# Kernel optimization log

Measured on AMD Instinct MI355X. Metric: run time of the kernel, lower is better.

## Reference

```python
import jax, jax.numpy as jnp
import numpy as np

N = 100000        # nodes
E = 1600000       # edges (N * avg_degree 16)
D_IN = 128
D_OUT = 32
OBS_T = 60        # observation_time -> decay table size 60*OBS_T = 3600
T_MAX = 60 * OBS_T


def setup_inputs() -> dict:
    key = jax.random.key(0)
    ks = jax.random.split(key, 8)
    inp = {
        "input": jax.random.normal(ks[0], (N, D_IN), dtype=jnp.float32),
        "W": jax.random.normal(ks[1], (D_IN, D_OUT), dtype=jnp.float32) * (np.sqrt(2.0) / np.sqrt(D_IN)),
        # decay weights are abs(normal(0, 0.02)) in the original; rand*0.04 is same scale
        "decay_weight1": jnp.abs(jax.random.normal(ks[2], (T_MAX, 1), dtype=jnp.float32) * 0.02),
        "decay_weight2": jnp.abs(jax.random.normal(ks[3], (T_MAX, 1), dtype=jnp.float32) * 0.02),
        "edge_row": jax.random.randint(ks[4], (E,), 0, N, dtype=jnp.int32),
        "edge_col": jax.random.randint(ks[5], (E,), 0, N, dtype=jnp.int32),
        # zero-based interval index; equals (adj_value - 1) of the original code
        "edge_time": jax.random.randint(ks[6], (E,), 0, T_MAX, dtype=jnp.int32),
        "arrive_time": jax.random.randint(ks[7], (N,), 0, T_MAX, dtype=jnp.int32),
        "observation_time": OBS_T,
    }
    return inp


def reference(input, W, decay_weight1, decay_weight2,
              edge_row, edge_col, edge_time, arrive_time, observation_time):
    n_nodes = input.shape[0]
    # h = relu(input @ W)  [N, D_OUT]
    h = jax.nn.relu(jnp.matmul(input, W))
    # one-hot(interval) @ decay_weight1 == embedding lookup  -> per-edge decay scalar
    decay = decay_weight1[edge_time, 0]                        # [E]
    # SpecialSpmm: out[i] = sum_{edges (i,j)} decay_e * h[j]  (gather-scale-scatter)
    msgs = decay[:, None] * h[edge_col]                        # [E, D_OUT]
    h_prime = jax.ops.segment_sum(msgs, edge_row, num_segments=n_nodes)
    # outlayer window decay: one-hot(60*T - arrive - 1) @ decay_weight2 == lookup
    win_idx = 60 * observation_time - arrive_time - 1          # [N] in [0, 60*T)
    h_prime = decay_weight2[win_idx, 0][:, None] * h_prime
    return h_prime
```

## Files before the change

### kernel.cpp

```cpp
#include <hip/hip_runtime.h>

#define N_NODES 100000
#define N_EDGES 1600000
#define D_IN    128
#define D_OUT   32
#define CROWS   2048
#define NCB     49
#define NSH     8
#define NSEG    (NCB * NSH)
#define CAP_A   4500
#define DEPTH   48
#define SEGSTRIDE 4608
#define SSTRIDE 2064
#define CAPW    1024
#define RPB3    32
#define K3_BLKS (NCB * 64)
#define GEMM_BLKS ((N_NODES + 63) / 64)
#define GEMM_A  782
#define GEMM_B  (GEMM_BLKS - GEMM_A)
#define GRID_A  2048
#define EPB_A   ((N_EDGES + GRID_A - 1) / GRID_A)

typedef __attribute__((ext_vector_type(8))) short bf16x8;
typedef __attribute__((ext_vector_type(4))) float f32x4;

__device__ inline short f2bf(float f) {
    union { float f; unsigned u; } v; v.f = f;
    unsigned r = (v.u + 0x7FFFu + ((v.u >> 16) & 1u)) >> 16;
    return (short)r;
}

__device__ inline void gemm_role(const float* __restrict__ input,
                                 const float* __restrict__ W,
                                 unsigned short* __restrict__ h16,
                                 short* wbt, int gblk, int tid)
{
    for (int i = tid; i < D_IN * D_OUT; i += 256) {
        const int k = i >> 5, c = i & 31;
        wbt[c * D_IN + k] = f2bf(W[i]);
    }
    __syncthreads();

    const int wave = tid >> 6;
    const int lane = tid & 63;
    const int r0   = gblk * 64 + wave * 16;
    const int c16  = lane & 15;
    const int quad = lane >> 4;

    int ra = r0 + c16;
    if (ra >= N_NODES) ra = N_NODES - 1;
    const float* arow = input + (size_t)ra * D_IN;

    f32x4 acc0 = {0.f, 0.f, 0.f, 0.f};
    f32x4 acc1 = {0.f, 0.f, 0.f, 0.f};
#pragma unroll
    for (int q = 0; q < 4; ++q) {
        const float* ap = arow + q * 32 + quad * 8;
        f32x4 a0 = *(const f32x4*)(ap);
        f32x4 a1 = *(const f32x4*)(ap + 4);
        bf16x8 af;
        af[0] = f2bf(a0.x); af[1] = f2bf(a0.y); af[2] = f2bf(a0.z); af[3] = f2bf(a0.w);
        af[4] = f2bf(a1.x); af[5] = f2bf(a1.y); af[6] = f2bf(a1.z); af[7] = f2bf(a1.w);
        bf16x8 b0 = *(const bf16x8*)(wbt + (c16)      * D_IN + q * 32 + quad * 8);
        bf16x8 b1 = *(const bf16x8*)(wbt + (c16 + 16) * D_IN + q * 32 + quad * 8);
        acc0 = __builtin_amdgcn_mfma_f32_16x16x32_bf16(af, b0, acc0, 0, 0, 0);
        acc1 = __builtin_amdgcn_mfma_f32_16x16x32_bf16(af, b1, acc1, 0, 0, 0);
    }
#pragma unroll
    for (int i = 0; i < 4; ++i) {
        const int rr = r0 + quad * 4 + i;
        if (rr < N_NODES) {
            h16[(size_t)rr * D_OUT + c16]      = (unsigned short)f2bf(fmaxf(acc0[i], 0.f));
            h16[(size_t)rr * D_OUT + c16 + 16] = (unsigned short)f2bf(fmaxf(acc1[i], 0.f));
        }
    }
}

union SMemPAG {
    struct { uint2 lbin[NCB][DEPTH]; int lcnt[NCB]; int gbase[NCB]; } a;
    struct { short wbt[D_IN * D_OUT]; } g;
};

__global__ __launch_bounds__(256) void phaseA_gemmA_kernel(
    const float* __restrict__ input, const float* __restrict__ W,
    const int* __restrict__ erow,    const int* __restrict__ ecol,
    const int* __restrict__ etime,
    unsigned short* __restrict__ h16,
    int* __restrict__ gcur,
    uint2* __restrict__ segA)
{
    __shared__ SMemPAG sm;
    const int tid = threadIdx.x;

    if (blockIdx.x < GRID_A) {
        const int blk   = blockIdx.x;
        const int shard = blk & (NSH - 1);
        const int wv    = tid >> 6;
        const int ln    = tid & 63;

        if (tid < NCB) sm.a.lcnt[tid] = 0;
        __syncthreads();

        const int e_beg = blk * EPB_A;
        const int e_end = min(e_beg + EPB_A, N_EDGES);

        for (int e = e_beg + tid; e < e_end; e += 256) {
            const int row = erow[e];
            const int cb  = row >> 11;
            uint2 p;
            p.x = (unsigned)ecol[e] | ((unsigned)(row & (CROWS - 1)) << 17);
            p.y = (unsigned)etime[e];
            const int pos = atomicAdd(&sm.a.lcnt[cb], 1);
            if (pos < DEPTH) sm.a.lbin[cb][pos] = p;
            else {
                const int gp = atomicAdd(&gcur[(cb * NSH + shard) * 16], 1);
                if (gp < CAP_A) segA[(size_t)(cb * NSH + shard) * CAP_A + gp] = p;
            }
        }
        __syncthreads();

        if (tid < NCB) {
            const int c = min(sm.a.lcnt[tid], DEPTH);
            sm.a.gbase[tid] = atomicAdd(&gcur[(tid * NSH + shard) * 16], c);
        }
        __syncthreads();

        for (int bin = wv; bin < NCB; bin += 4) {
            const int c  = min(sm.a.lcnt[bin], DEPTH);
            const int gb = sm.a.gbase[bin];
            uint2* seg = segA + (size_t)(bin * NSH + shard) * CAP_A;
            for (int k = ln; k < c; k += 64)
                if (gb + k < CAP_A) seg[gb + k] = sm.a.lbin[bin][k];
        }
    } else {
        gemm_role(input, W, h16, sm.g.wbt, blockIdx.x - GRID_A, tid);
    }
}

union SMemSSG {
    struct { int hist[CROWS]; int curs[CROWS]; int part[256]; } s;
    struct { short wbt[D_IN * D_OUT]; } g;
};

__global__ __launch_bounds__(256) void sortseg_gemmB_kernel(
    const float* __restrict__ input, const float* __restrict__ W,
    unsigned short* __restrict__ h16,
    const int* __restrict__ gcur, const uint2* __restrict__ segA,
    int* __restrict__ sseg, unsigned* __restrict__ spk2s)
{
    __shared__ SMemSSG sm;
    const int tid = threadIdx.x;

    if (blockIdx.x < NSEG) {
        const int b = blockIdx.x;
        const int n = min(gcur[b * 16], CAP_A);
        const uint2* seg = segA + (size_t)b * CAP_A;

        for (int t = tid; t < CROWS; t += 256) sm.s.hist[t] = 0;
        __syncthreads();

        for (int i = tid; i < n; i += 256)
            atomicAdd(&sm.s.hist[(seg[i].x >> 17) & (CROWS - 1)], 1);
        __syncthreads();

        int tmp[8]; int s0 = 0;
        const int base = tid * 8;
#pragma unroll
        for (int k = 0; k < 8; ++k) { tmp[k] = sm.s.hist[base + k]; s0 += tmp[k]; }
        sm.s.part[tid] = s0;
        __syncthreads();
        for (int off = 1; off < 256; off <<= 1) {
            int v = sm.s.part[tid];
            if (tid >= off) v += sm.s.part[tid - off];
            __syncthreads(); sm.s.part[tid] = v; __syncthreads();
        }
        int run = sm.s.part[tid] - s0;
#pragma unroll
        for (int k = 0; k < 8; ++k) { sm.s.curs[base + k] = run; run += tmp[k]; }
        __syncthreads();

        int* sg = sseg + (size_t)b * SSTRIDE;
        for (int t = tid; t < CROWS; t += 256) sg[t] = sm.s.curs[t];
        if (tid == 0) sg[CROWS] = n;
        __syncthreads();

        unsigned* dst = spk2s + (size_t)b * SEGSTRIDE;
        for (int i = tid; i < n; i += 256) {
            const uint2 p  = seg[i];
            const int   rl = (p.x >> 17) & (CROWS - 1);
            dst[atomicAdd(&sm.s.curs[rl], 1)] = (p.x & 0x1FFFFu) | (p.y << 20);
        }
    } else {
        gemm_role(input, W, h16, sm.g.wbt, GEMM_A + (int)blockIdx.x - NSEG, tid);
    }
}

__global__ __launch_bounds__(256) void merge_reduce_kernel(
    const unsigned short* __restrict__ h16, const int* __restrict__ sseg,
    const unsigned* __restrict__ spk2s,
    const float* __restrict__ dw1, const float* __restrict__ dw2,
    const int* __restrict__ arrive, const int* __restrict__ obs,
    float* __restrict__ out)
{
    __shared__ int ls8[NSH][RPB3 + 1];
    __shared__ int pre[NSH][RPB3];
    __shared__ int totL[RPB3];
    __shared__ int dstart[RPB3 + 1];
    __shared__ unsigned st[CAPW];

    const int b   = blockIdx.x;
    const int cb  = b >> 6;
    const int rl0 = (b & 63) * RPB3;
    const int g0  = cb * CROWS + rl0;
    if (g0 >= N_NODES) return;
    const int tid = threadIdx.x;

    for (int t = tid; t < NSH * (RPB3 + 1); t += 256) {
        const int s = t / (RPB3 + 1), i = t - s * (RPB3 + 1);
        ls8[s][i] = sseg[(size_t)(cb * NSH + s) * SSTRIDE + rl0 + i];
    }
    __syncthreads();

    if (tid < RPB3) {
        int accp = 0;
#pragma unroll
        for (int s = 0; s < NSH; ++s) {
            pre[s][tid] = accp;
            accp += ls8[s][tid + 1] - ls8[s][tid];
        }
        totL[tid] = accp;
    }
    __syncthreads();
    if (tid == 0) {
        int runp = 0;
#pragma unroll
        for (int r = 0; r < RPB3; ++r) { dstart[r] = runp; runp += totL[r]; }
        dstart[RPB3] = runp;
    }
    __syncthreads();

#pragma unroll
    for (int s = 0; s < NSH; ++s) {
        const int sb   = ls8[s][0];
        const int span = ls8[s][RPB3] - sb;
        const unsigned* src = spk2s + (size_t)(cb * NSH + s) * SEGSTRIDE;
        for (int i = tid; i < span; i += 256) {
            const int gidx = sb + i;
            int lo = 0, hi = RPB3 - 1;
#pragma unroll
            for (int it = 0; it < 5; ++it) {
                const int mid = (lo + hi + 1) >> 1;
                if (ls8[s][mid] <= gidx) lo = mid; else hi = mid - 1;
            }
            const int pos = dstart[lo] + pre[s][lo] + (gidx - ls8[s][lo]);
            if (pos < CAPW) st[pos] = src[gidx];
        }
    }
    __syncthreads();

    const int g  = tid >> 3;
    const int li = tid & 7;
    const int row = g0 + g;
    const int begc = min(dstart[g], CAPW);
    const int endc = min(dstart[g + 1], CAPW);
    const int n    = endc - begc;
    const unsigned* recs = &st[begc];
    const unsigned short* hp = h16 + li * 4;

    float a0 = 0.f, a1 = 0.f, a2 = 0.f, a3 = 0.f;
    int j = 0;
    for (; j + 8 <= n; j += 8) {
#pragma unroll
        for (int u = 0; u < 8; ++u) {
            const unsigned rec = recs[j + u];
            const uint2 hv = *(const uint2*)(hp + ((size_t)(rec & 0x1FFFFu) << 5));
            const float w  = dw1[rec >> 20];
            a0 = fmaf(w, __uint_as_float(hv.x << 16),         a0);
            a1 = fmaf(w, __uint_as_float(hv.x & 0xFFFF0000u), a1);
            a2 = fmaf(w, __uint_as_float(hv.y << 16),         a2);
            a3 = fmaf(w, __uint_as_float(hv.y & 0xFFFF0000u), a3);
        }
    }
    for (; j < n; ++j) {
        const unsigned rec = recs[j];
        const uint2 hv = *(const uint2*)(hp + ((size_t)(rec & 0x1FFFFu) << 5));
        const float w  = dw1[rec >> 20];
        a0 = fmaf(w, __uint_as_float(hv.x << 16),         a0);
        a1 = fmaf(w, __uint_as_float(hv.x & 0xFFFF0000u), a1);
        a2 = fmaf(w, __uint_as_float(hv.y << 16),         a2);
        a3 = fmaf(w, __uint_as_float(hv.y & 0xFFFF0000u), a3);
    }

    const int T = 60 * obs[0];
    const float sdw = dw2[T - arrive[row] - 1];
    float4 o;
    o.x = a0 * sdw; o.y = a1 * sdw; o.z = a2 * sdw; o.w = a3 * sdw;
    *(float4*)(out + ((size_t)row << 5) + li * 4) = o;
}

extern "C" void kernel_launch(void* const* d_in, const int* in_sizes, int n_in,
                              void* d_out, int out_size, void* d_ws, size_t ws_size,
                              hipStream_t stream)
{
    const float* input  = (const float*)d_in[0];
    const float* W      = (const float*)d_in[1];
    const float* dw1    = (const float*)d_in[2];
    const float* dw2    = (const float*)d_in[3];
    const int*   erow   = (const int*)d_in[4];
    const int*   ecol   = (const int*)d_in[5];
    const int*   etime  = (const int*)d_in[6];
    const int*   arrive = (const int*)d_in[7];
    const int*   obs    = (const int*)d_in[8];

    float* out = (float*)d_out;

    char* p = (char*)d_ws;
    unsigned short* h16 = (unsigned short*)p;
    p += (size_t)N_NODES * D_OUT * 2;
    p = (char*)(((size_t)p + 255) & ~(size_t)255);
    int* gcur = (int*)p;
    p += (size_t)NSEG * 16 * 4;
    p = (char*)(((size_t)p + 255) & ~(size_t)255);
    uint2* segA = (uint2*)p;
    p += (size_t)NSEG * CAP_A * 8;
    p = (char*)(((size_t)p + 255) & ~(size_t)255);
    unsigned* spk2s = (unsigned*)p;
    p += (size_t)NSEG * SEGSTRIDE * 4;
    p = (char*)(((size_t)p + 255) & ~(size_t)255);
    int* sseg = (int*)p;

    hipMemsetAsync(gcur, 0, (size_t)NSEG * 16 * 4, stream);

    phaseA_gemmA_kernel<<<GRID_A + GEMM_A, 256, 0, stream>>>(
        input, W, erow, ecol, etime, h16, gcur, segA);
    sortseg_gemmB_kernel<<<NSEG + GEMM_B, 256, 0, stream>>>(
        input, W, h16, gcur, segA, sseg, spk2s);
    merge_reduce_kernel<<<K3_BLKS, 256, 0, stream>>>(
        h16, sseg, spk2s, dw1, dw2, arrive, obs, out);
}
```

Measured before the change: 176.2 us.

## Fuse sort and merge kernels with per-chunk atomic readiness flags

All GEMM blocks now run in the first kernel alongside binning, instead of splitting the GEMM across two kernels. The sort and merge kernels are merged into one launch: sort blocks signal completion per column-block chunk with release atomics, and merge blocks spin-wait on those counters before consuming the sorted segments. This removes one kernel launch boundary and lets merging of ready chunks overlap with sorting of others. In exchange it relies on sort blocks being scheduled before the dependent merge blocks, which could deadlock if they were not, and the spinning burns CU slots.

New measurement: 649.2 us. +268.4%, slower.

```diff
diff --git a/kernel.cpp b/kernel.cpp
--- a/kernel.cpp
+++ b/kernel.cpp
@@ -14,10 +14,8 @@
 #define SSTRIDE 2064
 #define CAPW    1024
 #define RPB3    32
-#define K3_BLKS (NCB * 64)
+#define MERGE_BLKS (NCB * 64)
 #define GEMM_BLKS ((N_NODES + 63) / 64)
-#define GEMM_A  782
-#define GEMM_B  (GEMM_BLKS - GEMM_A)
 #define GRID_A  2048
 #define EPB_A   ((N_EDGES + GRID_A - 1) / GRID_A)
 
@@ -30,58 +28,12 @@
     return (short)r;
 }
 
-__device__ inline void gemm_role(const float* __restrict__ input,
-                                 const float* __restrict__ W,
-                                 unsigned short* __restrict__ h16,
-                                 short* wbt, int gblk, int tid)
-{
-    for (int i = tid; i < D_IN * D_OUT; i += 256) {
-        const int k = i >> 5, c = i & 31;
-        wbt[c * D_IN + k] = f2bf(W[i]);
-    }
-    __syncthreads();
-
-    const int wave = tid >> 6;
-    const int lane = tid & 63;
-    const int r0   = gblk * 64 + wave * 16;
-    const int c16  = lane & 15;
-    const int quad = lane >> 4;
-
-    int ra = r0 + c16;
-    if (ra >= N_NODES) ra = N_NODES - 1;
-    const float* arow = input + (size_t)ra * D_IN;
-
-    f32x4 acc0 = {0.f, 0.f, 0.f, 0.f};
-    f32x4 acc1 = {0.f, 0.f, 0.f, 0.f};
-#pragma unroll
-    for (int q = 0; q < 4; ++q) {
-        const float* ap = arow + q * 32 + quad * 8;
-        f32x4 a0 = *(const f32x4*)(ap);
-        f32x4 a1 = *(const f32x4*)(ap + 4);
-        bf16x8 af;
-        af[0] = f2bf(a0.x); af[1] = f2bf(a0.y); af[2] = f2bf(a0.z); af[3] = f2bf(a0.w);
-        af[4] = f2bf(a1.x); af[5] = f2bf(a1.y); af[6] = f2bf(a1.z); af[7] = f2bf(a1.w);
-        bf16x8 b0 = *(const bf16x8*)(wbt + (c16)      * D_IN + q * 32 + quad * 8);
-        bf16x8 b1 = *(const bf16x8*)(wbt + (c16 + 16) * D_IN + q * 32 + quad * 8);
-        acc0 = __builtin_amdgcn_mfma_f32_16x16x32_bf16(af, b0, acc0, 0, 0, 0);
-        acc1 = __builtin_amdgcn_mfma_f32_16x16x32_bf16(af, b1, acc1, 0, 0, 0);
-    }
-#pragma unroll
-    for (int i = 0; i < 4; ++i) {
-        const int rr = r0 + quad * 4 + i;
-        if (rr < N_NODES) {
-            h16[(size_t)rr * D_OUT + c16]      = (unsigned short)f2bf(fmaxf(acc0[i], 0.f));
-            h16[(size_t)rr * D_OUT + c16 + 16] = (unsigned short)f2bf(fmaxf(acc1[i], 0.f));
-        }
-    }
-}
-
-union SMemPAG {
+union SMemGA {
+    struct { short wbt[D_IN * D_OUT]; } g;
     struct { uint2 lbin[NCB][DEPTH]; int lcnt[NCB]; int gbase[NCB]; } a;
-    struct { short wbt[D_IN * D_OUT]; } g;
 };
 
-__global__ __launch_bounds__(256) void phaseA_gemmA_kernel(
+__global__ __launch_bounds__(256) void gemm_phaseA_kernel(
     const float* __restrict__ input, const float* __restrict__ W,
     const int* __restrict__ erow,    const int* __restrict__ ecol,
     const int* __restrict__ etime,
@@ -89,11 +41,51 @@
     int* __restrict__ gcur,
     uint2* __restrict__ segA)
 {
-    __shared__ SMemPAG sm;
+    __shared__ SMemGA sm;
     const int tid = threadIdx.x;
 
-    if (blockIdx.x < GRID_A) {
-        const int blk   = blockIdx.x;
+    if (blockIdx.x < GEMM_BLKS) {
+        for (int i = tid; i < D_IN * D_OUT; i += 256) {
+            const int k = i >> 5, c = i & 31;
+            sm.g.wbt[c * D_IN + k] = f2bf(W[i]);
+        }
+        __syncthreads();
+
+        const int wave = tid >> 6;
+        const int lane = tid & 63;
+        const int r0   = blockIdx.x * 64 + wave * 16;
+        const int c16  = lane & 15;
+        const int quad = lane >> 4;
+
+        int ra = r0 + c16;
+        if (ra >= N_NODES) ra = N_NODES - 1;
+        const float* arow = input + (size_t)ra * D_IN;
+
+        f32x4 acc0 = {0.f, 0.f, 0.f, 0.f};
+        f32x4 acc1 = {0.f, 0.f, 0.f, 0.f};
+#pragma unroll
+        for (int q = 0; q < 4; ++q) {
+            const float* ap = arow + q * 32 + quad * 8;
+            f32x4 a0 = *(const f32x4*)(ap);
+            f32x4 a1 = *(const f32x4*)(ap + 4);
+            bf16x8 af;
+            af[0] = f2bf(a0.x); af[1] = f2bf(a0.y); af[2] = f2bf(a0.z); af[3] = f2bf(a0.w);
+            af[4] = f2bf(a1.x); af[5] = f2bf(a1.y); af[6] = f2bf(a1.z); af[7] = f2bf(a1.w);
+            bf16x8 b0 = *(const bf16x8*)(sm.g.wbt + (c16)      * D_IN + q * 32 + quad * 8);
+            bf16x8 b1 = *(const bf16x8*)(sm.g.wbt + (c16 + 16) * D_IN + q * 32 + quad * 8);
+            acc0 = __builtin_amdgcn_mfma_f32_16x16x32_bf16(af, b0, acc0, 0, 0, 0);
+            acc1 = __builtin_amdgcn_mfma_f32_16x16x32_bf16(af, b1, acc1, 0, 0, 0);
+        }
+#pragma unroll
+        for (int i = 0; i < 4; ++i) {
+            const int rr = r0 + quad * 4 + i;
+            if (rr < N_NODES) {
+                h16[(size_t)rr * D_OUT + c16]      = (unsigned short)f2bf(fmaxf(acc0[i], 0.f));
+                h16[(size_t)rr * D_OUT + c16 + 16] = (unsigned short)f2bf(fmaxf(acc1[i], 0.f));
+            }
+        }
+    } else {
+        const int blk   = blockIdx.x - GEMM_BLKS;
         const int shard = blk & (NSH - 1);
         const int wv    = tid >> 6;
         const int ln    = tid & 63;
@@ -132,23 +124,25 @@
             for (int k = ln; k < c; k += 64)
                 if (gb + k < CAP_A) seg[gb + k] = sm.a.lbin[bin][k];
         }
-    } else {
-        gemm_role(input, W, h16, sm.g.wbt, blockIdx.x - GRID_A, tid);
     }
 }
 
-union SMemSSG {
+union SMemSM {
     struct { int hist[CROWS]; int curs[CROWS]; int part[256]; } s;
-    struct { short wbt[D_IN * D_OUT]; } g;
+    struct { int ls8[NSH][RPB3 + 1]; int pre[NSH][RPB3]; int totL[RPB3];
+             int dstart[RPB3 + 1]; unsigned st[CAPW]; } m;
 };
 
-__global__ __launch_bounds__(256) void sortseg_gemmB_kernel(
-    const float* __restrict__ input, const float* __restrict__ W,
-    unsigned short* __restrict__ h16,
+__global__ __launch_bounds__(256) void sort_merge_kernel(
+    const unsigned short* __restrict__ h16,
     const int* __restrict__ gcur, const uint2* __restrict__ segA,
-    int* __restrict__ sseg, unsigned* __restrict__ spk2s)
+    int* __restrict__ sseg, unsigned* __restrict__ spk2s,
+    int* __restrict__ segdone,
+    const float* __restrict__ dw1, const float* __restrict__ dw2,
+    const int* __restrict__ arrive, const int* __restrict__ obs,
+    float* __restrict__ out)
 {
-    __shared__ SMemSSG sm;
+    __shared__ SMemSM sm;
     const int tid = threadIdx.x;
 
     if (blockIdx.x < NSEG) {
@@ -190,89 +184,95 @@
             const int   rl = (p.x >> 17) & (CROWS - 1);
             dst[atomicAdd(&sm.s.curs[rl], 1)] = (p.x & 0x1FFFFu) | (p.y << 20);
         }
+        __syncthreads();
+
+        if (tid == 0) {
+            __threadfence();
+            __hip_atomic_fetch_add(&segdone[(b >> 3) * 16], 1,
+                                   __ATOMIC_RELEASE, __HIP_MEMORY_SCOPE_AGENT);
+        }
     } else {
-        gemm_role(input, W, h16, sm.g.wbt, GEMM_A + (int)blockIdx.x - NSEG, tid);
-    }
-}
-
-__global__ __launch_bounds__(256) void merge_reduce_kernel(
-    const unsigned short* __restrict__ h16, const int* __restrict__ sseg,
-    const unsigned* __restrict__ spk2s,
-    const float* __restrict__ dw1, const float* __restrict__ dw2,
-    const int* __restrict__ arrive, const int* __restrict__ obs,
-    float* __restrict__ out)
-{
-    __shared__ int ls8[NSH][RPB3 + 1];
-    __shared__ int pre[NSH][RPB3];
-    __shared__ int totL[RPB3];
-    __shared__ int dstart[RPB3 + 1];
-    __shared__ unsigned st[CAPW];
-
-    const int b   = blockIdx.x;
-    const int cb  = b >> 6;
-    const int rl0 = (b & 63) * RPB3;
-    const int g0  = cb * CROWS + rl0;
-    if (g0 >= N_NODES) return;
-    const int tid = threadIdx.x;
-
-    for (int t = tid; t < NSH * (RPB3 + 1); t += 256) {
-        const int s = t / (RPB3 + 1), i = t - s * (RPB3 + 1);
-        ls8[s][i] = sseg[(size_t)(cb * NSH + s) * SSTRIDE + rl0 + i];
-    }
-    __syncthreads();
-
-    if (tid < RPB3) {
-        int accp = 0;
+        const int b2  = blockIdx.x - NSEG;
+        const int cb  = b2 >> 6;
+        const int rl0 = (b2 & 63) * RPB3;
+        const int g0  = cb * CROWS + rl0;
+        if (g0 >= N_NODES) return;
+
+        if (tid == 0) {
+            while (__hip_atomic_load(&segdone[cb * 16], __ATOMIC_ACQUIRE,
+                                     __HIP_MEMORY_SCOPE_AGENT) < NSH)
+                __builtin_amdgcn_s_sleep(2);
+        }
+        __syncthreads();
+
+        for (int t = tid; t < NSH * (RPB3 + 1); t += 256) {
+            const int s = t / (RPB3 + 1), i = t - s * (RPB3 + 1);
+            sm.m.ls8[s][i] = sseg[(size_t)(cb * NSH + s) * SSTRIDE + rl0 + i];
+        }
+        __syncthreads();
+
+        if (tid < RPB3) {
+            int accp = 0;
+#pragma unroll
+            for (int s = 0; s < NSH; ++s) {
+                sm.m.pre[s][tid] = accp;
+                accp += sm.m.ls8[s][tid + 1] - sm.m.ls8[s][tid];
+            }
+            sm.m.totL[tid] = accp;
+        }
+        __syncthreads();
+        if (tid == 0) {
+            int runp = 0;
+#pragma unroll
+            for (int r = 0; r < RPB3; ++r) { sm.m.dstart[r] = runp; runp += sm.m.totL[r]; }
+            sm.m.dstart[RPB3] = runp;
+        }
+        __syncthreads();
+
 #pragma unroll
         for (int s = 0; s < NSH; ++s) {
-            pre[s][tid] = accp;
-            accp += ls8[s][tid + 1] - ls8[s][tid];
-        }
-        totL[tid] = accp;
-    }
-    __syncthreads();
-    if (tid == 0) {
-        int runp = 0;
-#pragma unroll
-        for (int r = 0; r < RPB3; ++r) { dstart[r] = runp; runp += totL[r]; }
-        dstart[RPB3] = runp;
-    }
-    __syncthreads();
-
-#pragma unroll
-    for (int s = 0; s < NSH; ++s) {
-        const int sb   = ls8[s][0];
-        const int span = ls8[s][RPB3] - sb;
-        const unsigned* src = spk2s + (size_t)(cb * NSH + s) * SEGSTRIDE;
-        for (int i = tid; i < span; i += 256) {
-            const int gidx = sb + i;
-            int lo = 0, hi = RPB3 - 1;
-#pragma unroll
-            for (int it = 0; it < 5; ++it) {
-                const int mid = (lo + hi + 1) >> 1;
-                if (ls8[s][mid] <= gidx) lo = mid; else hi = mid - 1;
-            }
-            const int pos = dstart[lo] + pre[s][lo] + (gidx - ls8[s][lo]);
-            if (pos < CAPW) st[pos] = src[gidx];
-        }
-    }
-    __syncthreads();
-
-    const int g  = tid >> 3;
-    const int li = tid & 7;
-    const int row = g0 + g;
-    const int begc = min(dstart[g], CAPW);
-    const int endc = min(dstart[g + 1], CAPW);
-    const int n    = endc - begc;
-    const unsigned* recs = &st[begc];
-    const unsigned short* hp = h16 + li * 4;
-
-    float a0 = 0.f, a1 = 0.f, a2 = 0.f, a3 = 0.f;
-    int j = 0;
-    for (; j + 8 <= n; j += 8) {
-#pragma unroll
-        for (int u = 0; u < 8; ++u) {
-            const unsigned rec = recs[j + u];
+            const int sb   = sm.m.ls8[s][0];
+            const int span = sm.m.ls8[s][RPB3] - sb;
+            const unsigned* src = spk2s + (size_t)(cb * NSH + s) * SEGSTRIDE;
+            for (int i = tid; i < span; i += 256) {
+                const int gidx = sb + i;
+                int lo = 0, hi = RPB3 - 1;
+#pragma unroll
+                for (int it = 0; it < 5; ++it) {
+                    const int mid = (lo + hi + 1) >> 1;
+                    if (sm.m.ls8[s][mid] <= gidx) lo = mid; else hi = mid - 1;
+                }
+                const int pos = sm.m.dstart[lo] + sm.m.pre[s][lo] + (gidx - sm.m.ls8[s][lo]);
+                if (pos < CAPW) sm.m.st[pos] = src[gidx];
+            }
+        }
+        __syncthreads();
+
+        const int g  = tid >> 3;
+        const int li = tid & 7;
+        const int row = g0 + g;
+        const int begc = min(sm.m.dstart[g], CAPW);
+        const int endc = min(sm.m.dstart[g + 1], CAPW);
+        const int n    = endc - begc;
+        const unsigned* recs = &sm.m.st[begc];
+        const unsigned short* hp = h16 + li * 4;
+
+        float a0 = 0.f, a1 = 0.f, a2 = 0.f, a3 = 0.f;
+        int j = 0;
+        for (; j + 8 <= n; j += 8) {
+#pragma unroll
+            for (int u = 0; u < 8; ++u) {
+                const unsigned rec = recs[j + u];
+                const uint2 hv = *(const uint2*)(hp + ((size_t)(rec & 0x1FFFFu) << 5));
+                const float w  = dw1[rec >> 20];
+                a0 = fmaf(w, __uint_as_float(hv.x << 16),         a0);
+                a1 = fmaf(w, __uint_as_float(hv.x & 0xFFFF0000u), a1);
+                a2 = fmaf(w, __uint_as_float(hv.y << 16),         a2);
+                a3 = fmaf(w, __uint_as_float(hv.y & 0xFFFF0000u), a3);
+            }
+        }
+        for (; j < n; ++j) {
+            const unsigned rec = recs[j];
             const uint2 hv = *(const uint2*)(hp + ((size_t)(rec & 0x1FFFFu) << 5));
             const float w  = dw1[rec >> 20];
             a0 = fmaf(w, __uint_as_float(hv.x << 16),         a0);
@@ -280,22 +280,13 @@
             a2 = fmaf(w, __uint_as_float(hv.y << 16),         a2);
             a3 = fmaf(w, __uint_as_float(hv.y & 0xFFFF0000u), a3);
         }
+
+        const int T = 60 * obs[0];
+        const float sdw = dw2[T - arrive[row] - 1];
+        float4 o;
+        o.x = a0 * sdw; o.y = a1 * sdw; o.z = a2 * sdw; o.w = a3 * sdw;
+        *(float4*)(out + ((size_t)row << 5) + li * 4) = o;
     }
-    for (; j < n; ++j) {
-        const unsigned rec = recs[j];
-        const uint2 hv = *(const uint2*)(hp + ((size_t)(rec & 0x1FFFFu) << 5));
-        const float w  = dw1[rec >> 20];
-        a0 = fmaf(w, __uint_as_float(hv.x << 16),         a0);
-        a1 = fmaf(w, __uint_as_float(hv.x & 0xFFFF0000u), a1);
-        a2 = fmaf(w, __uint_as_float(hv.y << 16),         a2);
-        a3 = fmaf(w, __uint_as_float(hv.y & 0xFFFF0000u), a3);
-    }
-
-    const int T = 60 * obs[0];
-    const float sdw = dw2[T - arrive[row] - 1];
-    float4 o;
-    o.x = a0 * sdw; o.y = a1 * sdw; o.z = a2 * sdw; o.w = a3 * sdw;
-    *(float4*)(out + ((size_t)row << 5) + li * 4) = o;
 }
 
 extern "C" void kernel_launch(void* const* d_in, const int* in_sizes, int n_in,
@@ -320,6 +311,8 @@
     p = (char*)(((size_t)p + 255) & ~(size_t)255);
     int* gcur = (int*)p;
     p += (size_t)NSEG * 16 * 4;
+    int* segdone = (int*)p;
+    p += (size_t)64 * 16 * 4;
     p = (char*)(((size_t)p + 255) & ~(size_t)255);
     uint2* segA = (uint2*)p;
     p += (size_t)NSEG * CAP_A * 8;
@@ -329,12 +322,10 @@
     p = (char*)(((size_t)p + 255) & ~(size_t)255);
     int* sseg = (int*)p;
 
-    hipMemsetAsync(gcur, 0, (size_t)NSEG * 16 * 4, stream);
-
-    phaseA_gemmA_kernel<<<GRID_A + GEMM_A, 256, 0, stream>>>(
+    hipMemsetAsync(gcur, 0, (size_t)(NSEG * 16 + 64 * 16) * 4, stream);
+
+    gemm_phaseA_kernel<<<GEMM_BLKS + GRID_A, 256, 0, stream>>>(
         input, W, erow, ecol, etime, h16, gcur, segA);
-    sortseg_gemmB_kernel<<<NSEG + GEMM_B, 256, 0, stream>>>(
-        input, W, h16, gcur, segA, sseg, spk2s);
-    merge_reduce_kernel<<<K3_BLKS, 256, 0, stream>>>(
-        h16, sseg, spk2s, dw1, dw2, arrive, obs, out);
+    sort_merge_kernel<<<NSEG + MERGE_BLKS, 256, 0, stream>>>(
+        h16, gcur, segA, sseg, spk2s, segdone, dw1, dw2, arrive, obs, out);
 }
```
